# Performance work log

Measured on AMD Instinct MI355X. Metric: run time of the kernel, lower is better.

Reference implementation:

```python
import jax, jax.numpy as jnp
import numpy as np

HIDDEN = 768
HEADS = 12
HEAD_DIM = HIDDEN // HEADS
NORM = float(np.sqrt(HIDDEN))  # module divides by sqrt(hidden_size), not sqrt(head_dim)


def setup_inputs() -> dict:
    key = jax.random.key(0)
    ks = jax.random.split(key, 7)
    B, S, H = 8, 1024, HIDDEN
    scale = 0.02
    return {
        "hidden_states": jax.random.normal(ks[0], (B, S, H), dtype=jnp.float32),
        "Wq": jax.random.normal(ks[1], (H, H), dtype=jnp.float32) * scale,
        "bq": jax.random.normal(ks[2], (H,), dtype=jnp.float32) * scale,
        "Wk": jax.random.normal(ks[3], (H, H), dtype=jnp.float32) * scale,
        "bk": jax.random.normal(ks[4], (H,), dtype=jnp.float32) * scale,
        "Wv": jax.random.normal(ks[5], (H, H), dtype=jnp.float32) * scale,
        "bv": jax.random.normal(ks[6], (H,), dtype=jnp.float32) * scale,
    }


def reference(hidden_states, Wq, bq, Wk, bk, Wv, bv):
    B, S, H = hidden_states.shape
    def heads(x):  # [B,S,H] -> [B,nh,S,hd]
        return x.reshape(B, S, HEADS, HEAD_DIM).transpose(0, 2, 1, 3)
    q = heads(hidden_states @ Wq + bq)
    k = heads(hidden_states @ Wk + bk)
    v = heads(hidden_states @ Wv + bv)
    # naive quadratic attention (world_size=1 ring): scores materialized
    scores = jnp.einsum("bhqd,bhkd->bhqk", q, k) / NORM
    probs = jax.nn.softmax(scores, axis=-1)  # dropout prob = 0.0
    ctx = jnp.einsum("bhqk,bhkd->bhqd", probs, v)
    # [B,nh,S,hd] -> [B,S,H]
    return ctx.transpose(0, 2, 1, 3).reshape(B, S, H)
```

## Files before the change

### kernel.cpp

```cpp
#include <hip/hip_runtime.h>
#include <hip/hip_bf16.h>
#include <stdint.h>

typedef __attribute__((ext_vector_type(8))) short short8;
typedef __attribute__((ext_vector_type(4))) float f32x4;
typedef __attribute__((ext_vector_type(4))) unsigned short u16x4;

#define HIDDEN 768
#define HEADS 12
#define HD 64
#define NB 8
#define SEQ 1024
#define MTOT (NB*SEQ)
#define QSCALE 0.05205887314427834f

typedef const __attribute__((address_space(1))) uint32_t* gas1_t;
typedef __attribute__((address_space(3))) uint32_t* las3_t;
#define GL_LDS16(g, l) __builtin_amdgcn_global_load_lds((gas1_t)(g), (las3_t)(l), 16, 0, 0)

static __device__ __forceinline__ unsigned short f2bf(float f){
  uint32_t u = __builtin_bit_cast(uint32_t, f);
  u += 0x7fffu + ((u >> 16) & 1u);
  return (unsigned short)(u >> 16);
}
static __device__ __forceinline__ unsigned short f2bf_hw(float f){
  return __builtin_bit_cast(unsigned short, __float2bfloat16(f));
}
static __device__ __forceinline__ float fexp2(float x){
#if __has_builtin(__builtin_amdgcn_exp2f)
  return __builtin_amdgcn_exp2f(x);
#else
  return exp2f(x);
#endif
}

#define DPP_STEP(x, ctrl, OP) { \
  int _t = __builtin_amdgcn_update_dpp(0, __builtin_bit_cast(int,(x)), (ctrl), 0xf, 0xf, true); \
  (x) = OP((x), __builtin_bit_cast(float,_t)); }
static __device__ __forceinline__ float addf(float a, float b){ return a+b; }
static __device__ __forceinline__ float dpp_sum16(float x){
  DPP_STEP(x, 0xB1, addf)
  DPP_STEP(x, 0x4E, addf)
  DPP_STEP(x, 0x141, addf)
  DPP_STEP(x, 0x140, addf)
  return x;
}

__global__ void convert_x_kernel(const float* __restrict__ x, unsigned short* __restrict__ xb){
  int i = blockIdx.x * 256 + threadIdx.x;
  float4 v = reinterpret_cast<const float4*>(x)[i];
  u16x4 o;
  o[0]=f2bf(v.x); o[1]=f2bf(v.y); o[2]=f2bf(v.z); o[3]=f2bf(v.w);
  reinterpret_cast<u16x4*>(xb)[i] = o;
}

__global__ void transpose_w_kernel(const float* __restrict__ Wq, const float* __restrict__ Wk,
                                   const float* __restrict__ Wv, unsigned short* __restrict__ Wt){
  __shared__ float t[32][33];
  int z = blockIdx.z;
  const float* W = (z==0) ? Wq : ((z==1) ? Wk : Wv);
  unsigned short* o = Wt + (size_t)z * HIDDEN * HIDDEN;
  int n0 = blockIdx.x * 32, k0 = blockIdx.y * 32;
  int x = threadIdx.x & 31, y0 = threadIdx.x >> 5;
#pragma unroll
  for(int p=0;p<4;p++){ int y = y0 + p*8; t[y][x] = W[(size_t)(k0+y)*HIDDEN + n0 + x]; }
  __syncthreads();
#pragma unroll
  for(int p=0;p<4;p++){ int y = y0 + p*8; o[(size_t)(n0+y)*HIDDEN + k0 + x] = f2bf(t[x][y]); }
}

__global__ __launch_bounds__(256, 4) void gemm_qkv_kernel(
    const unsigned short* __restrict__ Xb, const unsigned short* __restrict__ Wt,
    const float* __restrict__ bq, const float* __restrict__ bk, const float* __restrict__ bv,
    unsigned short* __restrict__ Qg, unsigned short* __restrict__ Kg, unsigned short* __restrict__ Vt)
{
  __shared__ alignas(16) unsigned short lA[128*64];
  __shared__ alignas(16) unsigned short lB[128*64];
  int wgid = blockIdx.x;
  int xcd = wgid & 7, idx = wgid >> 3;
  int y = xcd + 8*(idx/18);
  int within = idx % 18;
  int xb = within % 6, z = within / 6;
  const unsigned short* W = Wt + (size_t)z*HIDDEN*HIDDEN;
  const float* bias = (z==0) ? bq : ((z==1) ? bk : bv);
  int m0 = y * 128, n0 = xb * 128;
  int tid = threadIdx.x;
  int w = tid >> 6, lane = tid & 63, l16 = lane & 15, g = lane >> 4;
  int wm = w >> 1, wn = w & 1;
  f32x4 acc[4][4] = {};
  for(int kt=0; kt<HIDDEN; kt+=64){
    __syncthreads();
#pragma unroll
    for(int p=0;p<4;p++){
      int t2 = p*256 + tid;
      int r = t2 >> 3;
      int cb = (((t2 & 7) << 4) ^ ((r & 7) << 4));
      GL_LDS16(Xb + (size_t)(m0 + r)*HIDDEN + kt + (cb >> 1), lA + p*2048 + w*512);
      GL_LDS16(W  + (size_t)(n0 + r)*HIDDEN + kt + (cb >> 1), lB + p*2048 + w*512);
    }
    __syncthreads();
#pragma unroll
    for(int kk=0;kk<2;kk++){
      short8 af[4], bf[4];
#pragma unroll
      for(int i=0;i<4;i++){
        int row = wm*64 + i*16 + l16;
        af[i] = *reinterpret_cast<const short8*>(
            reinterpret_cast<const unsigned char*>(lA) + row*128 + ((kk*64 + g*16) ^ ((row&7)<<4)));
      }
#pragma unroll
      for(int j=0;j<4;j++){
        int row = wn*64 + j*16 + l16;
        bf[j] = *reinterpret_cast<const short8*>(
            reinterpret_cast<const unsigned char*>(lB) + row*128 + ((kk*64 + g*16) ^ ((row&7)<<4)));
      }
#pragma unroll
      for(int i=0;i<4;i++)
#pragma unroll
        for(int j=0;j<4;j++)
          acc[i][j] = __builtin_amdgcn_mfma_f32_16x16x32_bf16(af[i], bf[j], acc[i][j], 0, 0, 0);
    }
  }
  if(z == 2){
#pragma unroll
    for(int i=0;i<4;i++){
      int mb = m0 + wm*64 + i*16 + g*4;
      int b = mb >> 10, s = mb & 1023;
#pragma unroll
      for(int j=0;j<4;j++){
        int n = n0 + wn*64 + j*16 + l16;
        float bi = bias[n];
        int h = n >> 6, d = n & 63;
        u16x4 pk;
#pragma unroll
        for(int r=0;r<4;r++) pk[r] = f2bf(acc[i][j][r] + bi);
        *reinterpret_cast<u16x4*>(Vt + ((size_t)(b*HEADS + h)*HD + d)*SEQ + s) = pk;
      }
    }
  } else {
    unsigned short* out = (z==0) ? Qg : Kg;
#pragma unroll
    for(int i=0;i<4;i++){
      int mb = m0 + wm*64 + i*16 + g*4;
#pragma unroll
      for(int j=0;j<4;j++){
        int n = n0 + wn*64 + j*16 + l16;
        float bi = bias[n];
        int h = n >> 6, d = n & 63;
#pragma unroll
        for(int r=0;r<4;r++){
          int m = mb + r;
          int b = m >> 10, s = m & 1023;
          float cv = acc[i][j][r] + bi;
          if(z == 0) cv *= QSCALE;
          out[((size_t)(b*HEADS + h)*SEQ + s)*HD + d] = f2bf(cv);
        }
      }
    }
  }
}

__global__ __launch_bounds__(256, 3) void attn_kernel(
    const unsigned short* __restrict__ Qg, const unsigned short* __restrict__ Kg,
    const unsigned short* __restrict__ Vt, float* __restrict__ out)
{
  __shared__ alignas(16) unsigned short lK[2][64*64];
  __shared__ alignas(16) unsigned short lV[2][64*64];
  __shared__ alignas(16) unsigned short lP[8*16*72];
  int wgid = blockIdx.x;
  int xcd = wgid & 7, ix = wgid >> 3;
  int bh = xcd*12 + (ix >> 3), qb = ix & 7;
  int b = bh / HEADS, h = bh % HEADS;
  int tid = threadIdx.x, w = tid >> 6, lane = tid & 63, l16 = lane & 15, g = lane >> 4;

  const unsigned short* Qbase = Qg + ((size_t)bh*SEQ + qb*128 + w*32)*HD;
  short8 qA0 = *reinterpret_cast<const short8*>(Qbase + l16*HD + g*8);
  short8 qA1 = *reinterpret_cast<const short8*>(Qbase + l16*HD + 32 + g*8);
  short8 qB0 = *reinterpret_cast<const short8*>(Qbase + (16+l16)*HD + g*8);
  short8 qB1 = *reinterpret_cast<const short8*>(Qbase + (16+l16)*HD + 32 + g*8);

  f32x4 oacc[2][4] = {};
  float lpart[2][4] = {};

  int sw = (l16 & 7) << 4;
  int ro0 = l16*128 + ((g*16) ^ sw);
  int ro1 = l16*128 + ((64 + g*16) ^ sw);
  const unsigned char* lKb = reinterpret_cast<const unsigned char*>(&lK[0][0]);
  const unsigned char* lVb = reinterpret_cast<const unsigned char*>(&lV[0][0]);
  unsigned short* PwW = lP + (w*2)*1152 + (g*4)*72 + l16;
  const unsigned short* PwR = lP + (w*2)*1152 + l16*72 + g*8;

  int r0 = tid >> 3;
  int cb0 = (((tid & 7) << 4) ^ ((r0 & 7) << 4)) >> 1;
  const unsigned short* gK0 = Kg + (size_t)bh*SEQ*HD + r0*HD + cb0;
  const unsigned short* gV0 = Vt + (size_t)bh*HD*SEQ + r0*SEQ + cb0;

#define STAGE(B, t) do { \
    GL_LDS16(gK0 + (t)*4096,          &lK[B][0] + w*512); \
    GL_LDS16(gK0 + (t)*4096 + 2048,   &lK[B][0] + 2048 + w*512); \
    GL_LDS16(gV0 + (t)*64,            &lV[B][0] + w*512); \
    GL_LDS16(gV0 + (t)*64 + 32*SEQ,   &lV[B][0] + 2048 + w*512); \
  } while(0)

#define TILE(CUR, kt, HAS_NEXT) do { \
    if(HAS_NEXT) STAGE((CUR)^1, (kt)+1); \
    short8 kf[4][2]; \
    _Pragma("unroll") for(int j=0;j<4;j++){ \
      kf[j][0] = *reinterpret_cast<const short8*>(lKb + (CUR)*8192 + j*2048 + ro0); \
      kf[j][1] = *reinterpret_cast<const short8*>(lKb + (CUR)*8192 + j*2048 + ro1); } \
    f32x4 s0[4], s1[4]; \
    _Pragma("unroll") for(int j=0;j<4;j++){ \
      f32x4 zz = {}; \
      zz    = __builtin_amdgcn_mfma_f32_16x16x32_bf16(qA0, kf[j][0], zz, 0,0,0); \
      s0[j] = __builtin_amdgcn_mfma_f32_16x16x32_bf16(qA1, kf[j][1], zz, 0,0,0); } \
    _Pragma("unroll") for(int j=0;j<4;j++){ \
      f32x4 zz = {}; \
      zz    = __builtin_amdgcn_mfma_f32_16x16x32_bf16(qB0, kf[j][0], zz, 0,0,0); \
      s1[j] = __builtin_amdgcn_mfma_f32_16x16x32_bf16(qB1, kf[j][1], zz, 0,0,0); } \
    float pv0[4][4], pv1[4][4]; \
    _Pragma("unroll") for(int r=0;r<4;r++){ \
      _Pragma("unroll") for(int j=0;j<4;j++) pv0[j][r] = fexp2(s0[j][r]); \
      lpart[0][r] += (pv0[0][r]+pv0[1][r])+(pv0[2][r]+pv0[3][r]); } \
    _Pragma("unroll") for(int r=0;r<4;r++){ \
      _Pragma("unroll") for(int j=0;j<4;j++) pv1[j][r] = fexp2(s1[j][r]); \
      lpart[1][r] += (pv1[0][r]+pv1[1][r])+(pv1[2][r]+pv1[3][r]); } \
    _Pragma("unroll") for(int r=0;r<4;r++){ \
      _Pragma("unroll") for(int j=0;j<4;j++){ \
        PwW[r*72 + j*16]        = f2bf_hw(pv0[j][r]); \
        PwW[1152 + r*72 + j*16] = f2bf_hw(pv1[j][r]); } } \
    asm volatile("" ::: "memory");   \
    short8 vf[4][2]; \
    _Pragma("unroll") for(int j=0;j<4;j++){ \
      vf[j][0] = *reinterpret_cast<const short8*>(lVb + (CUR)*8192 + j*2048 + ro0); \
      vf[j][1] = *reinterpret_cast<const short8*>(lVb + (CUR)*8192 + j*2048 + ro1); } \
    { short8 pa0 = *reinterpret_cast<const short8*>(PwR); \
      short8 pa1 = *reinterpret_cast<const short8*>(PwR + 32); \
      _Pragma("unroll") for(int jn=0;jn<4;jn++){ \
        oacc[0][jn] = __builtin_amdgcn_mfma_f32_16x16x32_bf16(pa0, vf[jn][0], oacc[0][jn], 0,0,0); \
        oacc[0][jn] = __builtin_amdgcn_mfma_f32_16x16x32_bf16(pa1, vf[jn][1], oacc[0][jn], 0,0,0); } } \
    { short8 pa0 = *reinterpret_cast<const short8*>(PwR + 1152); \
      short8 pa1 = *reinterpret_cast<const short8*>(PwR + 1152 + 32); \
      _Pragma("unroll") for(int jn=0;jn<4;jn++){ \
        oacc[1][jn] = __builtin_amdgcn_mfma_f32_16x16x32_bf16(pa0, vf[jn][0], oacc[1][jn], 0,0,0); \
        oacc[1][jn] = __builtin_amdgcn_mfma_f32_16x16x32_bf16(pa1, vf[jn][1], oacc[1][jn], 0,0,0); } } \
    __syncthreads(); \
  } while(0)

  STAGE(0, 0);
  __syncthreads();

  for(int kt=0; kt<SEQ/64; kt+=2){
    TILE(0, kt, true);
    TILE(1, kt+1, (kt+1) < SEQ/64 - 1);
  }

#pragma unroll
  for(int rg=0;rg<2;rg++)
#pragma unroll
  for(int r=0;r<4;r++){
    int s = qb*128 + w*32 + rg*16 + g*4 + r;
    float invl = 1.0f / dpp_sum16(lpart[rg][r]);
    float* orow = out + ((size_t)b*SEQ + s)*HIDDEN + h*HD;
#pragma unroll
    for(int jn=0;jn<4;jn++) orow[jn*16 + l16] = oacc[rg][jn][r] * invl;
  }
#undef STAGE
#undef TILE
}

extern "C" void kernel_launch(void* const* d_in, const int* in_sizes, int n_in,
                              void* d_out, int out_size, void* d_ws, size_t ws_size,
                              hipStream_t stream) {
  const float* hs = (const float*)d_in[0];
  const float* Wq = (const float*)d_in[1];
  const float* bq = (const float*)d_in[2];
  const float* Wk = (const float*)d_in[3];
  const float* bk = (const float*)d_in[4];
  const float* Wv = (const float*)d_in[5];
  const float* bv = (const float*)d_in[6];
  float* out = (float*)d_out;

  char* ws = (char*)d_ws;
  unsigned short* Xb = (unsigned short*)ws;
  unsigned short* Wt = (unsigned short*)(ws + (size_t)12582912);
  unsigned short* Qg = (unsigned short*)(ws + (size_t)16121856);
  unsigned short* Kg = Qg + (size_t)MTOT*HIDDEN;
  unsigned short* Vt = Kg + (size_t)MTOT*HIDDEN;

  convert_x_kernel<<<MTOT*HIDDEN/4/256, 256, 0, stream>>>(hs, Xb);
  transpose_w_kernel<<<dim3(24,24,3), 256, 0, stream>>>(Wq, Wk, Wv, Wt);
  gemm_qkv_kernel<<<1152, 256, 0, stream>>>(Xb, Wt, bq, bk, bv, Qg, Kg, Vt);
  attn_kernel<<<768, 256, 0, stream>>>(Qg, Kg, Vt, out);
}
```

Before: 92.61 us.

## Keep softmax probabilities in registers by transposing S=K·Qᵀ MFMA layout

The QK^T product is computed with K as the A operand, so each lane holds scores for one query row across keys. The exponentiated probabilities can then be packed with v_cvt_pk_bf16_f32 and fed straight into the PV MFMA as the B operand, with no LDS round trip. V fragments are read as two 8-byte LDS loads per operand to match this layout. The row-sum reduction becomes two cross-lane shuffles instead of a DPP chain, and outputs are written as float4. This removes the lP shared buffer and its writes and reads, but uses narrower V LDS reads and relies on the operand layout being correct.

```diff
diff --git a/kernel.cpp b/kernel.cpp
--- a/kernel.cpp
+++ b/kernel.cpp
@@ -4,6 +4,8 @@
 
 typedef __attribute__((ext_vector_type(8))) short short8;
 typedef __attribute__((ext_vector_type(4))) float f32x4;
+typedef __attribute__((ext_vector_type(4))) int i32x4;
+typedef __attribute__((ext_vector_type(2))) int i32x2;
 typedef __attribute__((ext_vector_type(4))) unsigned short u16x4;
 
 #define HIDDEN 768
@@ -23,27 +25,12 @@
   u += 0x7fffu + ((u >> 16) & 1u);
   return (unsigned short)(u >> 16);
 }
-static __device__ __forceinline__ unsigned short f2bf_hw(float f){
-  return __builtin_bit_cast(unsigned short, __float2bfloat16(f));
-}
 static __device__ __forceinline__ float fexp2(float x){
 #if __has_builtin(__builtin_amdgcn_exp2f)
   return __builtin_amdgcn_exp2f(x);
 #else
   return exp2f(x);
 #endif
-}
-
-#define DPP_STEP(x, ctrl, OP) { \
-  int _t = __builtin_amdgcn_update_dpp(0, __builtin_bit_cast(int,(x)), (ctrl), 0xf, 0xf, true); \
-  (x) = OP((x), __builtin_bit_cast(float,_t)); }
-static __device__ __forceinline__ float addf(float a, float b){ return a+b; }
-static __device__ __forceinline__ float dpp_sum16(float x){
-  DPP_STEP(x, 0xB1, addf)
-  DPP_STEP(x, 0x4E, addf)
-  DPP_STEP(x, 0x141, addf)
-  DPP_STEP(x, 0x140, addf)
-  return x;
 }
 
 __global__ void convert_x_kernel(const float* __restrict__ x, unsigned short* __restrict__ xb){
@@ -166,7 +153,6 @@
 {
   __shared__ alignas(16) unsigned short lK[2][64*64];
   __shared__ alignas(16) unsigned short lV[2][64*64];
-  __shared__ alignas(16) unsigned short lP[8*16*72];
   int wgid = blockIdx.x;
   int xcd = wgid & 7, ix = wgid >> 3;
   int bh = xcd*12 + (ix >> 3), qb = ix & 7;
@@ -180,15 +166,17 @@
   short8 qB1 = *reinterpret_cast<const short8*>(Qbase + (16+l16)*HD + 32 + g*8);
 
   f32x4 oacc[2][4] = {};
-  float lpart[2][4] = {};
+  float lpart[2] = {0.f, 0.f};
 
   int sw = (l16 & 7) << 4;
   int ro0 = l16*128 + ((g*16) ^ sw);
   int ro1 = l16*128 + ((64 + g*16) ^ sw);
+  int vo00 = l16*128 + ((      8*g) ^ sw);
+  int vo01 = l16*128 + ((32  + 8*g) ^ sw);
+  int vo10 = l16*128 + ((64  + 8*g) ^ sw);
+  int vo11 = l16*128 + ((96  + 8*g) ^ sw);
   const unsigned char* lKb = reinterpret_cast<const unsigned char*>(&lK[0][0]);
   const unsigned char* lVb = reinterpret_cast<const unsigned char*>(&lV[0][0]);
-  unsigned short* PwW = lP + (w*2)*1152 + (g*4)*72 + l16;
-  const unsigned short* PwR = lP + (w*2)*1152 + l16*72 + g*8;
 
   int r0 = tid >> 3;
   int cb0 = (((tid & 7) << 4) ^ ((r0 & 7) << 4)) >> 1;
@@ -202,47 +190,48 @@
     GL_LDS16(gV0 + (t)*64 + 32*SEQ,   &lV[B][0] + 2048 + w*512); \
   } while(0)
 
+#define SMPV(SREG, LP, OA) do { \
+    int Wlo[4], Whi[4]; \
+    _Pragma("unroll") for(int j=0;j<4;j++){ \
+      float p0=fexp2(SREG[j][0]), p1=fexp2(SREG[j][1]); \
+      float p2=fexp2(SREG[j][2]), p3=fexp2(SREG[j][3]); \
+      LP += (p0+p1)+(p2+p3); \
+      asm("v_cvt_pk_bf16_f32 %0, %1, %2" : "=v"(Wlo[j]) : "v"(p0), "v"(p1)); \
+      asm("v_cvt_pk_bf16_f32 %0, %1, %2" : "=v"(Whi[j]) : "v"(p2), "v"(p3)); } \
+    _Pragma("unroll") for(int m=0;m<2;m++){ \
+      i32x4 cc; cc[0]=Wlo[2*m]; cc[1]=Whi[2*m]; cc[2]=Wlo[2*m+1]; cc[3]=Whi[2*m+1]; \
+      short8 pB = __builtin_bit_cast(short8, cc); \
+      _Pragma("unroll") for(int jn=0;jn<4;jn++) \
+        OA[jn] = __builtin_amdgcn_mfma_f32_16x16x32_bf16(vf[jn][m], pB, OA[jn], 0,0,0); } \
+  } while(0)
+
 #define TILE(CUR, kt, HAS_NEXT) do { \
     if(HAS_NEXT) STAGE((CUR)^1, (kt)+1); \
     short8 kf[4][2]; \
     _Pragma("unroll") for(int j=0;j<4;j++){ \
       kf[j][0] = *reinterpret_cast<const short8*>(lKb + (CUR)*8192 + j*2048 + ro0); \
       kf[j][1] = *reinterpret_cast<const short8*>(lKb + (CUR)*8192 + j*2048 + ro1); } \
+    short8 vf[4][2]; \
+    _Pragma("unroll") for(int jn=0;jn<4;jn++){ \
+      { i32x2 vl = *reinterpret_cast<const i32x2*>(lVb + (CUR)*8192 + jn*2048 + vo00); \
+        i32x2 vh = *reinterpret_cast<const i32x2*>(lVb + (CUR)*8192 + jn*2048 + vo01); \
+        i32x4 vc; vc[0]=vl[0]; vc[1]=vl[1]; vc[2]=vh[0]; vc[3]=vh[1]; \
+        vf[jn][0] = __builtin_bit_cast(short8, vc); } \
+      { i32x2 vl = *reinterpret_cast<const i32x2*>(lVb + (CUR)*8192 + jn*2048 + vo10); \
+        i32x2 vh = *reinterpret_cast<const i32x2*>(lVb + (CUR)*8192 + jn*2048 + vo11); \
+        i32x4 vc; vc[0]=vl[0]; vc[1]=vl[1]; vc[2]=vh[0]; vc[3]=vh[1]; \
+        vf[jn][1] = __builtin_bit_cast(short8, vc); } } \
     f32x4 s0[4], s1[4]; \
     _Pragma("unroll") for(int j=0;j<4;j++){ \
       f32x4 zz = {}; \
-      zz    = __builtin_amdgcn_mfma_f32_16x16x32_bf16(qA0, kf[j][0], zz, 0,0,0); \
-      s0[j] = __builtin_amdgcn_mfma_f32_16x16x32_bf16(qA1, kf[j][1], zz, 0,0,0); } \
+      zz    = __builtin_amdgcn_mfma_f32_16x16x32_bf16(kf[j][0], qA0, zz, 0,0,0); \
+      s0[j] = __builtin_amdgcn_mfma_f32_16x16x32_bf16(kf[j][1], qA1, zz, 0,0,0); } \
     _Pragma("unroll") for(int j=0;j<4;j++){ \
       f32x4 zz = {}; \
-      zz    = __builtin_amdgcn_mfma_f32_16x16x32_bf16(qB0, kf[j][0], zz, 0,0,0); \
-      s1[j] = __builtin_amdgcn_mfma_f32_16x16x32_bf16(qB1, kf[j][1], zz, 0,0,0); } \
-    float pv0[4][4], pv1[4][4]; \
-    _Pragma("unroll") for(int r=0;r<4;r++){ \
-      _Pragma("unroll") for(int j=0;j<4;j++) pv0[j][r] = fexp2(s0[j][r]); \
-      lpart[0][r] += (pv0[0][r]+pv0[1][r])+(pv0[2][r]+pv0[3][r]); } \
-    _Pragma("unroll") for(int r=0;r<4;r++){ \
-      _Pragma("unroll") for(int j=0;j<4;j++) pv1[j][r] = fexp2(s1[j][r]); \
-      lpart[1][r] += (pv1[0][r]+pv1[1][r])+(pv1[2][r]+pv1[3][r]); } \
-    _Pragma("unroll") for(int r=0;r<4;r++){ \
-      _Pragma("unroll") for(int j=0;j<4;j++){ \
-        PwW[r*72 + j*16]        = f2bf_hw(pv0[j][r]); \
-        PwW[1152 + r*72 + j*16] = f2bf_hw(pv1[j][r]); } } \
-    asm volatile("" ::: "memory");   \
-    short8 vf[4][2]; \
-    _Pragma("unroll") for(int j=0;j<4;j++){ \
-      vf[j][0] = *reinterpret_cast<const short8*>(lVb + (CUR)*8192 + j*2048 + ro0); \
-      vf[j][1] = *reinterpret_cast<const short8*>(lVb + (CUR)*8192 + j*2048 + ro1); } \
-    { short8 pa0 = *reinterpret_cast<const short8*>(PwR); \
-      short8 pa1 = *reinterpret_cast<const short8*>(PwR + 32); \
-      _Pragma("unroll") for(int jn=0;jn<4;jn++){ \
-        oacc[0][jn] = __builtin_amdgcn_mfma_f32_16x16x32_bf16(pa0, vf[jn][0], oacc[0][jn], 0,0,0); \
-        oacc[0][jn] = __builtin_amdgcn_mfma_f32_16x16x32_bf16(pa1, vf[jn][1], oacc[0][jn], 0,0,0); } } \
-    { short8 pa0 = *reinterpret_cast<const short8*>(PwR + 1152); \
-      short8 pa1 = *reinterpret_cast<const short8*>(PwR + 1152 + 32); \
-      _Pragma("unroll") for(int jn=0;jn<4;jn++){ \
-        oacc[1][jn] = __builtin_amdgcn_mfma_f32_16x16x32_bf16(pa0, vf[jn][0], oacc[1][jn], 0,0,0); \
-        oacc[1][jn] = __builtin_amdgcn_mfma_f32_16x16x32_bf16(pa1, vf[jn][1], oacc[1][jn], 0,0,0); } } \
+      zz    = __builtin_amdgcn_mfma_f32_16x16x32_bf16(kf[j][0], qB0, zz, 0,0,0); \
+      s1[j] = __builtin_amdgcn_mfma_f32_16x16x32_bf16(kf[j][1], qB1, zz, 0,0,0); } \
+    SMPV(s0, lpart[0], oacc[0]); \
+    SMPV(s1, lpart[1], oacc[1]); \
     __syncthreads(); \
   } while(0)
 
@@ -255,16 +244,23 @@
   }
 
 #pragma unroll
-  for(int rg=0;rg<2;rg++)
-#pragma unroll
-  for(int r=0;r<4;r++){
-    int s = qb*128 + w*32 + rg*16 + g*4 + r;
-    float invl = 1.0f / dpp_sum16(lpart[rg][r]);
-    float* orow = out + ((size_t)b*SEQ + s)*HIDDEN + h*HD;
-#pragma unroll
-    for(int jn=0;jn<4;jn++) orow[jn*16 + l16] = oacc[rg][jn][r] * invl;
+  for(int rg=0;rg<2;rg++){
+    float tot = lpart[rg];
+    tot += __shfl_xor(tot, 16, 64);
+    tot += __shfl_xor(tot, 32, 64);
+    float invl = 1.0f / tot;
+    int s = qb*128 + w*32 + rg*16 + l16;
+    float* orow = out + ((size_t)b*SEQ + s)*HIDDEN + h*HD + 4*g;
+#pragma unroll
+    for(int jn=0;jn<4;jn++){
+      float4 val;
+      val.x = oacc[rg][jn][0]*invl; val.y = oacc[rg][jn][1]*invl;
+      val.z = oacc[rg][jn][2]*invl; val.w = oacc[rg][jn][3]*invl;
+      *reinterpret_cast<float4*>(orow + 16*jn) = val;
+    }
   }
 #undef STAGE
+#undef SMPV
 #undef TILE
 }
 
```

New measurement: 88.23 us. 4.7% less time.
